# Optimization experiments

Measured on AMD Instinct MI355X. Metric: run time of the kernel, lower is better.

Reference implementation:

```python
import jax, jax.numpy as jnp
import numpy as np

P, H_OUT, D, NX = 32, 1, 256, 16
S_A = -0.1

def layernorm(x, g, b, eps=1e-5):
    mu = jnp.mean(x, axis=-1, keepdims=True)
    var = jnp.var(x, axis=-1, keepdims=True)
    return (x - mu) * jax.lax.rsqrt(var + eps) * g + b

def setup_inputs() -> dict:
    key = jax.random.key(0)
    ks = jax.random.split(key, 16)
    B, L = 8, 2048
    y = jax.random.normal(ks[0], (B, L, P), jnp.float32)
    Win = jax.random.normal(ks[1], (P, D), jnp.float32) / np.sqrt(P)
    bin_ = jnp.zeros((D,), jnp.float32)
    ng = jnp.ones((D,), jnp.float32); nb = jnp.zeros((D,), jnp.float32)
    # A = -10*rand + s_A, with A[:,0] = s_A (fix first state of each channel)
    A = -10.0 * jax.random.uniform(ks[2], (D, NX), jnp.float32) + S_A
    A = A.at[:, 0].set(S_A)
    W_B = jax.random.normal(ks[3], (NX, D), jnp.float32)
    W_C = jax.random.normal(ks[4], (NX, D), jnp.float32)
    q_delta = jax.random.normal(ks[5], (D,), jnp.float32)
    p_delta = jax.random.normal(ks[6], (1,), jnp.float32)
    nfg = jnp.ones((D,), jnp.float32); nfb = jnp.zeros((D,), jnp.float32)
    W1 = jax.random.normal(ks[7], (D, D), jnp.float32) / np.sqrt(D)
    b1 = jnp.zeros((D,), jnp.float32)
    W2 = jax.random.normal(ks[8], (D, H_OUT * P), jnp.float32) / np.sqrt(D)
    b2 = jnp.zeros((H_OUT * P,), jnp.float32)
    return {"y": y, "Win": Win, "bin_": bin_, "ng": ng, "nb": nb, "A": A,
            "W_B": W_B, "W_C": W_C, "q_delta": q_delta, "p_delta": p_delta,
            "nfg": nfg, "nfb": nfb, "W1": W1, "b1": b1, "W2": W2, "b2": b2}

def selective_scan(u, delta, A, Bm, Cm):
    # u: (B,L,D), delta: (B,L), A: (D,NX), Bm/Cm: (B,L,NX)
    dA = jnp.exp(delta[..., None, None] * A)                      # (B,L,D,NX)
    dBu = delta[..., None, None] * Bm[:, :, None, :] * u[..., None]  # (B,L,D,NX)
    x0 = jnp.zeros((u.shape[0], u.shape[2], A.shape[1]), u.dtype)
    def step(x, inp):
        dA_t, dBu_t, C_t = inp
        x = dA_t * x + dBu_t                                      # (B,D,NX)
        y_t = jnp.einsum('bdn,bn->bd', x, C_t)
        return x, y_t
    _, ys = jax.lax.scan(step, x0, (dA.transpose(1, 0, 2, 3),
                                    dBu.transpose(1, 0, 2, 3),
                                    Cm.transpose(1, 0, 2)))
    return ys.transpose(1, 0, 2)                                  # (B,L,D)

def reference(y, Win, bin_, ng, nb, A, W_B, W_C, q_delta, p_delta,
              nfg, nfb, W1, b1, W2, b2):
    B, L, _ = y.shape
    h = y @ Win + bin_                                            # (B,L,D)
    hn = layernorm(h, ng, nb)
    delta = jax.nn.softplus(p_delta[0] + jnp.einsum('bld,d->bl', hn, q_delta))
    Bm = jnp.einsum('nd,bld->bln', W_B, hn)
    Cm = jnp.einsum('nd,bld->bln', W_C, hn)
    upd = selective_scan(hn, delta, A, Bm, Cm)
    h = h + upd
    h = layernorm(h, nfg, nfb)
    out = jax.nn.gelu(h @ W1 + b1, approximate=False) @ W2 + b2
    return out.reshape(B, L, H_OUT, P)
```

## Files before the change

### kernel.cpp

```cpp
#include <hip/hip_runtime.h>
#include <math.h>

#define D 256
#define NX 16
#define L 2048
#define NBATCH 8
#define NTOK (NBATCH * L)
#define CL 32
#define NCH (L / CL)
#define LOG2E 1.44269504088896340736f

typedef float f32x4 __attribute__((ext_vector_type(4)));
typedef short bf16x8 __attribute__((ext_vector_type(8)));

__device__ __forceinline__ unsigned short f2bf(float x) {
  unsigned u = __float_as_uint(x);
  u = u + 0x7fffu + ((u >> 16) & 1u);
  return (unsigned short)(u >> 16);
}
__device__ __forceinline__ float bf2f(unsigned short h) {
  return __uint_as_float(((unsigned)h) << 16);
}

__global__ __launch_bounds__(256) void k0_prep(const float* __restrict__ A,
                                               const float* __restrict__ WB,
                                               const float* __restrict__ WC,
                                               const float* __restrict__ Win,
                                               const float* __restrict__ W1,
                                               const float* __restrict__ W2,
                                               float* __restrict__ At,
                                               unsigned short* __restrict__ W1fh,
                                               unsigned short* __restrict__ W1fl,
                                               unsigned short* __restrict__ W2fh,
                                               unsigned short* __restrict__ W2fl,
                                               unsigned short* __restrict__ Winfh,
                                               unsigned short* __restrict__ Winfl,
                                               unsigned short* __restrict__ Wbcfh,
                                               unsigned short* __restrict__ Wbcfl) {
  int i = blockIdx.x * 256 + threadIdx.x;
  if (i < 4096) {
    int d = i >> 4, n = i & 15;
    At[n * D + d] = A[i] * LOG2E;
  } else if (i < 12288) {
    int e = i - 4096;
    int j = e & 7, l = (e >> 3) & 63, tt = e >> 9;
    int k = ((l >> 4) << 3) + j;
    int n = tt * 16 + (l & 15);
    float x = Win[k * 256 + n];
    unsigned short h = f2bf(x);
    Winfh[e] = h;
    Winfl[e] = f2bf(x - bf2f(h));
  } else if (i < 20480) {
    int e = i - 12288;
    int j = e & 7, l = (e >> 3) & 63, q = e >> 9;
    int s = q >> 1, tt = q & 1;
    int k = s * 32 + ((l >> 4) << 3) + j;
    int n = tt * 16 + (l & 15);
    float x = (n < 16) ? WB[n * 256 + k] : WC[(n - 16) * 256 + k];
    unsigned short h = f2bf(x);
    Wbcfh[e] = h;
    Wbcfl[e] = f2bf(x - bf2f(h));
  } else if (i < 86016) {
    int e = i - 20480;
    int j = e & 7, l = (e >> 3) & 63, tt = (e >> 9) & 15, s = e >> 13;
    int k = s * 32 + ((l >> 4) << 3) + j;
    int n = tt * 16 + (l & 15);
    float x = W1[k * 256 + n];
    unsigned short h = f2bf(x);
    W1fh[e] = h;
    W1fl[e] = f2bf(x - bf2f(h));
  } else {
    int e = i - 86016;
    int j = e & 7, l = (e >> 3) & 63, tt = (e >> 9) & 1, s = e >> 10;
    int k = s * 32 + ((l >> 4) << 3) + j;
    int n = tt * 16 + (l & 15);
    float x = W2[k * 32 + n];
    unsigned short h = f2bf(x);
    W2fh[e] = h;
    W2fl[e] = f2bf(x - bf2f(h));
  }
}

__global__ __launch_bounds__(512, 4) void k1a_front_scan(
    const float* __restrict__ y, const float* __restrict__ bin_,
    const float* __restrict__ ng, const float* __restrict__ nb,
    const float* __restrict__ qd, const float* __restrict__ pd,
    const float* __restrict__ At,
    const unsigned short* __restrict__ Winfh,
    const unsigned short* __restrict__ Winfl,
    const unsigned short* __restrict__ Wbcfh,
    const unsigned short* __restrict__ Wbcfl,
    float* __restrict__ hn, float* __restrict__ delta,
    float* __restrict__ Bm, float* __restrict__ Cm,
    float* __restrict__ muv, float* __restrict__ irsv,
    float* __restrict__ EX, float* __restrict__ T) {
  __shared__ float sy[32][36];
  __shared__ float sh[32][260];
  __shared__ float sB[32][NX];
  __shared__ float sred[32][16];
  __shared__ float sdelta[32];
  __shared__ float smu[32];
  __shared__ float srstd[32];
  __shared__ __align__(16) unsigned short sChA_h[32 * 256];
  __shared__ __align__(16) unsigned short sChA_l[32 * 256];
  int t = threadIdx.x;
  int l = t & 63;
  int w = t >> 6;
  int tok0 = blockIdx.x * 32;
  if (t < 256) {
    int row = t >> 3, c4 = t & 7;
    *(float4*)&sy[row][c4 * 4] = ((const float4*)(y + (size_t)tok0 * 32))[t];
  }
  __syncthreads();
  f32x4 acc[2][2];
  {
    bf16x8 yah[2], yal[2];
    int k0 = (l >> 4) << 3;
    #pragma unroll
    for (int m = 0; m < 2; ++m) {
      int row = m * 16 + (l & 15);
      float4 f0 = *(float4*)&sy[row][k0];
      float4 f1 = *(float4*)&sy[row][k0 + 4];
      float v0 = f0.x, v1_ = f0.y, v2 = f0.z, v3 = f0.w;
      float v4 = f1.x, v5 = f1.y, v6 = f1.z, v7 = f1.w;
      unsigned short h0 = f2bf(v0), h1 = f2bf(v1_), h2 = f2bf(v2), h3 = f2bf(v3);
      unsigned short h4 = f2bf(v4), h5 = f2bf(v5), h6 = f2bf(v6), h7 = f2bf(v7);
      yah[m][0] = (short)h0; yah[m][1] = (short)h1; yah[m][2] = (short)h2; yah[m][3] = (short)h3;
      yah[m][4] = (short)h4; yah[m][5] = (short)h5; yah[m][6] = (short)h6; yah[m][7] = (short)h7;
      yal[m][0] = (short)f2bf(v0 - bf2f(h0)); yal[m][1] = (short)f2bf(v1_ - bf2f(h1));
      yal[m][2] = (short)f2bf(v2 - bf2f(h2)); yal[m][3] = (short)f2bf(v3 - bf2f(h3));
      yal[m][4] = (short)f2bf(v4 - bf2f(h4)); yal[m][5] = (short)f2bf(v5 - bf2f(h5));
      yal[m][6] = (short)f2bf(v6 - bf2f(h6)); yal[m][7] = (short)f2bf(v7 - bf2f(h7));
    }
    const bf16x8* Bh = (const bf16x8*)Winfh;
    const bf16x8* Bl = (const bf16x8*)Winfl;
    #pragma unroll
    for (int n = 0; n < 2; ++n) {
      int tt = w * 2 + n;
      bf16x8 bh = Bh[tt * 64 + l];
      bf16x8 bl = Bl[tt * 64 + l];
      #pragma unroll
      for (int m = 0; m < 2; ++m) {
        f32x4 a = {0.f, 0.f, 0.f, 0.f};
        a = __builtin_amdgcn_mfma_f32_16x16x32_bf16(yah[m], bh, a, 0, 0, 0);
        a = __builtin_amdgcn_mfma_f32_16x16x32_bf16(yal[m], bh, a, 0, 0, 0);
        a = __builtin_amdgcn_mfma_f32_16x16x32_bf16(yah[m], bl, a, 0, 0, 0);
        a = __builtin_amdgcn_mfma_f32_16x16x32_bf16(yal[m], bl, a, 0, 0, 0);
        acc[m][n] = a;
      }
    }
  }
  int c0 = w * 32 + (l & 15), c1 = c0 + 16;
  {
    float b0 = bin_[c0], b1v = bin_[c1];
    #pragma unroll
    for (int m = 0; m < 2; ++m)
      #pragma unroll
      for (int r = 0; r < 4; ++r) { acc[m][0][r] += b0; acc[m][1][r] += b1v; }
  }
  {
    #pragma unroll
    for (int m = 0; m < 2; ++m)
      #pragma unroll
      for (int r = 0; r < 4; ++r) {
        float a0 = acc[m][0][r], a1 = acc[m][1][r];
        float s1 = a0 + a1;
        float s2 = a0 * a0 + a1 * a1;
        #pragma unroll
        for (int off = 1; off < 16; off <<= 1) {
          s1 += __shfl_xor(s1, off);
          s2 += __shfl_xor(s2, off);
        }
        if ((l & 15) == 0) {
          int tok = m * 16 + ((l >> 4) << 2) + r;
          sred[tok][w * 2] = s1;
          sred[tok][w * 2 + 1] = s2;
        }
      }
  }
  __syncthreads();
  if (t < 32) {
    float s1 = 0.f, s2 = 0.f;
    #pragma unroll
    for (int q = 0; q < 8; ++q) { s1 += sred[t][q * 2]; s2 += sred[t][q * 2 + 1]; }
    float mu = s1 * (1.f / D);
    float var = s2 * (1.f / D) - mu * mu;
    float rstd = rsqrtf(var + 1e-5f);
    smu[t] = mu;
    srstd[t] = rstd;
    muv[tok0 + t] = mu;
    irsv[tok0 + t] = sqrtf(var + 1e-5f);
  }
  __syncthreads();
  {
    float g0 = ng[c0], g1 = ng[c1];
    float nb0 = nb[c0], nb1 = nb[c1];
    float q0 = qd[c0], q1 = qd[c1];
    float ddv[2][4];
    #pragma unroll
    for (int m = 0; m < 2; ++m)
      #pragma unroll
      for (int r = 0; r < 4; ++r) {
        int tok = m * 16 + ((l >> 4) << 2) + r;
        float mu = smu[tok], rstd = srstd[tok];
        float h0 = (acc[m][0][r] - mu) * rstd * g0 + nb0;
        float h1 = (acc[m][1][r] - mu) * rstd * g1 + nb1;
        sh[tok][c0] = h0;
        sh[tok][c1] = h1;
        float dx = h0 * q0 + h1 * q1;
        #pragma unroll
        for (int off = 1; off < 16; off <<= 1) dx += __shfl_xor(dx, off);
        ddv[m][r] = dx;
      }
    if ((l & 15) == 0) {
      #pragma unroll
      for (int m = 0; m < 2; ++m)
        #pragma unroll
        for (int r = 0; r < 4; ++r)
          sred[m * 16 + ((l >> 4) << 2) + r][w] = ddv[m][r];
    }
  }
  __syncthreads();
  if (t < 32) {
    float dsum = 0.f;
    #pragma unroll
    for (int q = 0; q < 8; ++q) dsum += sred[t][q];
    float xx = pd[0] + dsum;
    float dv = (xx > 20.f) ? xx : log1pf(expf(xx));
    delta[tok0 + t] = dv;
    sdelta[t] = dv;
    float tv = dv;
    #pragma unroll
    for (int off = 1; off < 32; off <<= 1) tv += __shfl_xor(tv, off);
    if (t == 0) T[blockIdx.x] = tv;
  }
  {
    int row = t & 31;
    int cq = (t >> 5) * 16;
    float4 f0 = *(float4*)&sh[row][cq];
    float4 f1 = *(float4*)&sh[row][cq + 4];
    float4 f2 = *(float4*)&sh[row][cq + 8];
    float4 f3 = *(float4*)&sh[row][cq + 12];
    float vv[16] = {f0.x, f0.y, f0.z, f0.w, f1.x, f1.y, f1.z, f1.w,
                    f2.x, f2.y, f2.z, f2.w, f3.x, f3.y, f3.z, f3.w};
    unsigned hw[8], lw[8];
    #pragma unroll
    for (int p = 0; p < 8; ++p) {
      unsigned short ha = f2bf(vv[2 * p]), hb = f2bf(vv[2 * p + 1]);
      unsigned short la = f2bf(vv[2 * p] - bf2f(ha));
      unsigned short lb = f2bf(vv[2 * p + 1] - bf2f(hb));
      hw[p] = (unsigned)ha | ((unsigned)hb << 16);
      lw[p] = (unsigned)la | ((unsigned)lb << 16);
    }
    unsigned base = (unsigned)row * 512;
    #pragma unroll
    for (int g = 0; g < 2; ++g) {
      unsigned off = ((unsigned)(cq * 2 + g * 16)) ^ ((unsigned)(row & 7) << 4);
      uint4 hv4 = {hw[g * 4], hw[g * 4 + 1], hw[g * 4 + 2], hw[g * 4 + 3]};
      uint4 lv4 = {lw[g * 4], lw[g * 4 + 1], lw[g * 4 + 2], lw[g * 4 + 3]};
      *(uint4*)((char*)sChA_h + base + off) = hv4;
      *(uint4*)((char*)sChA_l + base + off) = lv4;
    }
  }
  __syncthreads();
  if (w < 4) {
    int mw = w & 1, nw = w >> 1;
    int row = mw * 16 + (l & 15);
    unsigned abase = (unsigned)row * 512;
    const bf16x8* B2h = (const bf16x8*)Wbcfh;
    const bf16x8* B2l = (const bf16x8*)Wbcfl;
    f32x4 acc2 = {0.f, 0.f, 0.f, 0.f};
    #pragma unroll
    for (int s = 0; s < 8; ++s) {
      unsigned off = ((unsigned)(s * 64 + ((l >> 4) << 4))) ^ ((unsigned)(row & 7) << 4);
      bf16x8 ah = *(const bf16x8*)((const char*)sChA_h + abase + off);
      bf16x8 al = *(const bf16x8*)((const char*)sChA_l + abase + off);
      int bi = (s * 2 + nw) * 64 + l;
      bf16x8 bh = B2h[bi];
      bf16x8 bl = B2l[bi];
      acc2 = __builtin_amdgcn_mfma_f32_16x16x32_bf16(ah, bh, acc2, 0, 0, 0);
      acc2 = __builtin_amdgcn_mfma_f32_16x16x32_bf16(al, bh, acc2, 0, 0, 0);
      acc2 = __builtin_amdgcn_mfma_f32_16x16x32_bf16(ah, bl, acc2, 0, 0, 0);
      acc2 = __builtin_amdgcn_mfma_f32_16x16x32_bf16(al, bl, acc2, 0, 0, 0);
    }
    int tokr = mw * 16 + ((l >> 4) << 2);
    int colc = l & 15;
    if (nw == 0) {
      #pragma unroll
      for (int r = 0; r < 4; ++r) {
        Bm[(size_t)(tok0 + tokr + r) * NX + colc] = acc2[r];
        sB[tokr + r][colc] = acc2[r];
      }
    } else {
      #pragma unroll
      for (int r = 0; r < 4; ++r)
        Cm[(size_t)(tok0 + tokr + r) * NX + colc] = acc2[r];
    }
  } else {
    float4* dst = (float4*)(hn + (size_t)tok0 * D);
    for (int i = t - 256; i < 2048; i += 256) {
      int row = i >> 6, c4 = i & 63;
      dst[i] = *(float4*)&sh[row][c4 * 4];
    }
  }
  __syncthreads();
  {
    int half = t >> 8;
    int d = t & 255;
    float a8[8], x8[8];
    #pragma unroll
    for (int n = 0; n < 8; ++n) {
      a8[n] = At[(half * 8 + n) * D + d];
      x8[n] = 0.f;
    }
    for (int lo = 0; lo < CL; ++lo) {
      float dlt = sdelta[lo];
      float du = dlt * sh[lo][d];
      float Bv[8];
      *(float4*)&Bv[0] = *(float4*)&sB[lo][half * 8];
      *(float4*)&Bv[4] = *(float4*)&sB[lo][half * 8 + 4];
      #pragma unroll
      for (int n = 0; n < 8; ++n)
        x8[n] = fmaf(exp2f(dlt * a8[n]), x8[n], du * Bv[n]);
    }
    size_t exbase = (size_t)blockIdx.x * (NX * D) + d;
    #pragma unroll
    for (int n = 0; n < 8; ++n) EX[exbase + (half * 8 + n) * D] = x8[n];
  }
}

__global__ __launch_bounds__(64) void k2b_chunkscan(
    const float* __restrict__ At, const float* __restrict__ T,
    float* __restrict__ EX) {
  __shared__ float sT[NCH];
  int b = blockIdx.x >> 6;
  int rem = ((blockIdx.x & 63) << 6) | threadIdx.x;
  sT[threadIdx.x] = T[b * NCH + threadIdx.x];
  __syncthreads();
  float A2 = At[rem];
  size_t base = ((size_t)b << 18) + rem;
  float eq[8];
  #pragma unroll
  for (int j = 0; j < 8; ++j) eq[j] = EX[base + ((size_t)j << 12)];
  float x = 0.f;
  #pragma unroll 8
  for (int c = 0; c < NCH; ++c) {
    float e = eq[c & 7];
    if (c + 8 < NCH) eq[c & 7] = EX[base + ((size_t)(c + 8) << 12)];
    EX[base + ((size_t)c << 12)] = x;
    x = fmaf(exp2f(sT[c] * A2), x, e);
  }
}

__device__ __forceinline__ float gelu_exact(float x) {
  return 0.5f * x * (1.f + erff(x * 0.70710678118654752440f));
}

__global__ __launch_bounds__(256) void k2cd_scan_mlp(
    const float* __restrict__ hn, const float* __restrict__ delta,
    const float* __restrict__ Bm, const float* __restrict__ Cm,
    const float* __restrict__ At, const float* __restrict__ EX,
    const float* __restrict__ muv, const float* __restrict__ irsv,
    const float* __restrict__ ng, const float* __restrict__ nb,
    const float* __restrict__ nfg, const float* __restrict__ nfb,
    const unsigned short* __restrict__ W1fh, const unsigned short* __restrict__ W1fl,
    const unsigned short* __restrict__ W2fh, const unsigned short* __restrict__ W2fl,
    const float* __restrict__ b1, const float* __restrict__ b2,
    float* __restrict__ out) {
  __shared__ float s_az[32 * 260];
  __shared__ __align__(16) unsigned short sAh[32 * 256];
  __shared__ __align__(16) unsigned short sAl[32 * 256];
  __shared__ float sB[32][NX];
  __shared__ float sC[32][NX];
  __shared__ float sdelta[32];
  __shared__ float smu[32];
  __shared__ float sirs[32];
  int t = threadIdx.x;
  int tok0 = blockIdx.x * 32;
  size_t tokbase = (size_t)tok0;
  if (t < 32) {
    sdelta[t] = delta[tokbase + t];
    smu[t] = muv[tokbase + t];
    sirs[t] = irsv[tokbase + t];
  }
  for (int i = t; i < 32 * NX; i += 256) {
    ((float*)sB)[i] = Bm[tokbase * NX + i];
    ((float*)sC)[i] = Cm[tokbase * NX + i];
  }
  float a16[16], x16[16];
  size_t exbase = (size_t)blockIdx.x * (NX * D) + t;
  #pragma unroll
  for (int n = 0; n < 16; ++n) {
    a16[n] = At[n * D + t];
    x16[n] = EX[exbase + n * D];
  }
  float nb_d = nb[t];
  float invg = 1.0f / ng[t];
  __syncthreads();
  {
    float hv = hn[tokbase * D + t];
    for (int lo = 0; lo < CL; ++lo) {
      float hv_next = (lo + 1 < CL) ? hn[(tokbase + lo + 1) * D + t] : 0.f;
      float dlt = sdelta[lo];
      float du = dlt * hv;
      float Bv[16], Cv[16];
      *(float4*)&Bv[0]  = *(float4*)&sB[lo][0];
      *(float4*)&Bv[4]  = *(float4*)&sB[lo][4];
      *(float4*)&Bv[8]  = *(float4*)&sB[lo][8];
      *(float4*)&Bv[12] = *(float4*)&sB[lo][12];
      *(float4*)&Cv[0]  = *(float4*)&sC[lo][0];
      *(float4*)&Cv[4]  = *(float4*)&sC[lo][4];
      *(float4*)&Cv[8]  = *(float4*)&sC[lo][8];
      *(float4*)&Cv[12] = *(float4*)&sC[lo][12];
      float p = 0.f;
      #pragma unroll
      for (int n = 0; n < 16; ++n) {
        x16[n] = fmaf(exp2f(dlt * a16[n]), x16[n], du * Bv[n]);
        p = fmaf(x16[n], Cv[n], p);
      }
      float h = fmaf((hv - nb_d) * invg, sirs[lo], smu[lo]);
      s_az[lo * 260 + t] = h + p;
      hv = hv_next;
    }
  }
  __syncthreads();
  int dcol = t & 63, jrow = t >> 6;
  int d4 = dcol * 4, j8 = jrow * 8;
  {
    float4 g4 = ((const float4*)nfg)[dcol];
    float4 b4 = ((const float4*)nfb)[dcol];
    for (int jj = 0; jj < 8; ++jj) {
      int lo = j8 + jj;
      float4 v = *(float4*)&s_az[lo * 260 + d4];
      float s1 = v.x + v.y + v.z + v.w;
      float s2 = v.x * v.x + v.y * v.y + v.z * v.z + v.w * v.w;
      #pragma unroll
      for (int off = 1; off < 64; off <<= 1) {
        s1 += __shfl_xor(s1, off);
        s2 += __shfl_xor(s2, off);
      }
      float mu2 = s1 * (1.f / D);
      float var2 = s2 * (1.f / D) - mu2 * mu2;
      float rstd2 = rsqrtf(var2 + 1e-5f);
      float4 o;
      o.x = (v.x - mu2) * rstd2 * g4.x + b4.x;
      o.y = (v.y - mu2) * rstd2 * g4.y + b4.y;
      o.z = (v.z - mu2) * rstd2 * g4.z + b4.z;
      o.w = (v.w - mu2) * rstd2 * g4.w + b4.w;
      unsigned short h0 = f2bf(o.x), h1 = f2bf(o.y), h2 = f2bf(o.z), h3 = f2bf(o.w);
      unsigned short q0 = f2bf(o.x - bf2f(h0));
      unsigned short q1 = f2bf(o.y - bf2f(h1));
      unsigned short q2 = f2bf(o.z - bf2f(h2));
      unsigned short q3 = f2bf(o.w - bf2f(h3));
      unsigned off16 = ((unsigned)(d4 * 2)) ^ ((unsigned)(lo & 7) << 4);
      uint2 hv2, lv2;
      hv2.x = (unsigned)h0 | ((unsigned)h1 << 16);
      hv2.y = (unsigned)h2 | ((unsigned)h3 << 16);
      lv2.x = (unsigned)q0 | ((unsigned)q1 << 16);
      lv2.y = (unsigned)q2 | ((unsigned)q3 << 16);
      *(uint2*)((char*)sAh + lo * 512 + off16) = hv2;
      *(uint2*)((char*)sAl + lo * 512 + off16) = lv2;
    }
  }
  __syncthreads();
  int l = t & 63, w = t >> 6;
  const bf16x8* B1h = (const bf16x8*)W1fh;
  const bf16x8* B1l = (const bf16x8*)W1fl;
  f32x4 acc[2][4];
  #pragma unroll
  for (int m = 0; m < 2; ++m)
    #pragma unroll
    for (int n = 0; n < 4; ++n) {
      f32x4 z4 = {0.f, 0.f, 0.f, 0.f};
      acc[m][n] = z4;
    }
  #pragma unroll 2
  for (int s = 0; s < 8; ++s) {
    bf16x8 ah[2], al[2];
    #pragma unroll
    for (int m = 0; m < 2; ++m) {
      int row = m * 16 + (l & 15);
      unsigned off16 = ((unsigned)(s * 64 + ((l >> 4) << 4))) ^ ((unsigned)(row & 7) << 4);
      ah[m] = *(const bf16x8*)((const char*)sAh + row * 512 + off16);
      al[m] = *(const bf16x8*)((const char*)sAl + row * 512 + off16);
    }
    #pragma unroll
    for (int n = 0; n < 4; ++n) {
      int bi = (s * 16 + w * 4 + n) * 64 + l;
      bf16x8 bh = B1h[bi];
      bf16x8 bl = B1l[bi];
      #pragma unroll
      for (int m = 0; m < 2; ++m) {
        acc[m][n] = __builtin_amdgcn_mfma_f32_16x16x32_bf16(ah[m], bh, acc[m][n], 0, 0, 0);
        acc[m][n] = __builtin_amdgcn_mfma_f32_16x16x32_bf16(al[m], bh, acc[m][n], 0, 0, 0);
        acc[m][n] = __builtin_amdgcn_mfma_f32_16x16x32_bf16(ah[m], bl, acc[m][n], 0, 0, 0);
        acc[m][n] = __builtin_amdgcn_mfma_f32_16x16x32_bf16(al[m], bl, acc[m][n], 0, 0, 0);
      }
    }
  }
  __syncthreads();
  #pragma unroll
  for (int n = 0; n < 4; ++n) {
    int colz = w * 64 + n * 16 + (l & 15);
    float b1v = b1[colz];
    #pragma unroll
    for (int m = 0; m < 2; ++m) {
      #pragma unroll
      for (int r = 0; r < 4; ++r) {
        int row = m * 16 + ((l >> 4) << 2) + r;
        float zv = gelu_exact(acc[m][n][r] + b1v);
        unsigned short zh = f2bf(zv);
        unsigned short zl = f2bf(zv - bf2f(zh));
        unsigned off16 = ((unsigned)(colz * 2)) ^ ((unsigned)(row & 7) << 4);
        *(unsigned short*)((char*)sAh + row * 512 + off16) = zh;
        *(unsigned short*)((char*)sAl + row * 512 + off16) = zl;
      }
    }
  }
  __syncthreads();
  int mw = w >> 1, nw = w & 1;
  const bf16x8* B2h = (const bf16x8*)W2fh;
  const bf16x8* B2l = (const bf16x8*)W2fl;
  f32x4 acc2 = {0.f, 0.f, 0.f, 0.f};
  #pragma unroll 2
  for (int s = 0; s < 8; ++s) {
    int row = mw * 16 + (l & 15);
    unsigned off16 = ((unsigned)(s * 64 + ((l >> 4) << 4))) ^ ((unsigned)(row & 7) << 4);
    bf16x8 zh8 = *(const bf16x8*)((const char*)sAh + row * 512 + off16);
    bf16x8 zl8 = *(const bf16x8*)((const char*)sAl + row * 512 + off16);
    int bi = (s * 2 + nw) * 64 + l;
    bf16x8 bh = B2h[bi];
    bf16x8 bl = B2l[bi];
    acc2 = __builtin_amdgcn_mfma_f32_16x16x32_bf16(zh8, bh, acc2, 0, 0, 0);
    acc2 = __builtin_amdgcn_mfma_f32_16x16x32_bf16(zl8, bh, acc2, 0, 0, 0);
    acc2 = __builtin_amdgcn_mfma_f32_16x16x32_bf16(zh8, bl, acc2, 0, 0, 0);
    acc2 = __builtin_amdgcn_mfma_f32_16x16x32_bf16(zl8, bl, acc2, 0, 0, 0);
  }
  int colo = nw * 16 + (l & 15);
  float b2v = b2[colo];
  #pragma unroll
  for (int r = 0; r < 4; ++r) {
    int row = mw * 16 + ((l >> 4) << 2) + r;
    out[(size_t)(tok0 + row) * 32 + colo] = acc2[r] + b2v;
  }
}

extern "C" void kernel_launch(void* const* d_in, const int* in_sizes, int n_in,
                              void* d_out, int out_size, void* d_ws, size_t ws_size,
                              hipStream_t stream) {
  const float* y    = (const float*)d_in[0];
  const float* Win  = (const float*)d_in[1];
  const float* bin_ = (const float*)d_in[2];
  const float* ng   = (const float*)d_in[3];
  const float* nb   = (const float*)d_in[4];
  const float* A    = (const float*)d_in[5];
  const float* WB   = (const float*)d_in[6];
  const float* WC   = (const float*)d_in[7];
  const float* qd   = (const float*)d_in[8];
  const float* pd   = (const float*)d_in[9];
  const float* nfg  = (const float*)d_in[10];
  const float* nfb  = (const float*)d_in[11];
  const float* W1   = (const float*)d_in[12];
  const float* b1   = (const float*)d_in[13];
  const float* W2   = (const float*)d_in[14];
  const float* b2   = (const float*)d_in[15];

  float* ws = (float*)d_ws;
  float* hnbuf = ws;
  float* delta = ws + 4194304;
  float* Bm    = delta + NTOK;
  float* Cm    = Bm + NTOK * NX;
  float* muv   = Cm + NTOK * NX;
  float* irsv  = muv + NTOK;
  float* Tbuf  = irsv + NTOK;
  float* At    = Tbuf + NBATCH * NCH;
  float* EX    = At + D * NX;
  unsigned short* W1fh  = (unsigned short*)(EX + 2097152);
  unsigned short* W1fl  = W1fh + 65536;
  unsigned short* W2fh  = W1fl + 65536;
  unsigned short* W2fl  = W2fh + 8192;
  unsigned short* Winfh = W2fl + 8192;
  unsigned short* Winfl = Winfh + 8192;
  unsigned short* Wbcfh = Winfl + 8192;
  unsigned short* Wbcfl = Wbcfh + 8192;

  k0_prep<<<368, 256, 0, stream>>>(A, WB, WC, Win, W1, W2, At,
                                   W1fh, W1fl, W2fh, W2fl,
                                   Winfh, Winfl, Wbcfh, Wbcfl);
  k1a_front_scan<<<NTOK / 32, 512, 0, stream>>>(y, bin_, ng, nb, qd, pd, At,
                                                Winfh, Winfl, Wbcfh, Wbcfl,
                                                hnbuf, delta, Bm, Cm,
                                                muv, irsv, EX, Tbuf);
  k2b_chunkscan<<<NBATCH * 64, 64, 0, stream>>>(At, Tbuf, EX);
  k2cd_scan_mlp<<<NTOK / 32, 256, 0, stream>>>(hnbuf, delta, Bm, Cm, At, EX,
                                               muv, irsv, ng, nb, nfg, nfb,
                                               W1fh, W1fl, W2fh, W2fl,
                                               b1, b2, (float*)d_out);
}
```

Baseline: 185.3 us.

## Split scan+MLP kernel into 16-token half-chunks using mid-chunk partial states

The front kernel now also writes the intra-chunk scan state after 16 tokens (EXmid) and a prefix sum of delta up to token 15 (cds15). The scan+MLP kernel runs on 16-token half-chunks, so it launches twice as many blocks, each with half the serial scan length. The second half reconstructs its starting state from the chunk carry plus the mid-chunk partial. This is meant to shorten the serial per-block scan and raise occupancy (launch bounds 256,4). In exchange it adds an extra 8MB EXmid write and read, duplicates the A/EX loads across two blocks, and leaves two of the four waves idle in the second GEMM.

Measured after the change: 180.8 us (median of 2 runs). 2.4% less time.

```diff
diff --git a/kernel.cpp b/kernel.cpp
--- a/kernel.cpp
+++ b/kernel.cpp
@@ -93,7 +93,8 @@
     float* __restrict__ hn, float* __restrict__ delta,
     float* __restrict__ Bm, float* __restrict__ Cm,
     float* __restrict__ muv, float* __restrict__ irsv,
-    float* __restrict__ EX, float* __restrict__ T) {
+    float* __restrict__ EX, float* __restrict__ EXmid,
+    float* __restrict__ cds15g, float* __restrict__ T) {
   __shared__ float sy[32][36];
   __shared__ float sh[32][260];
   __shared__ float sB[32][NX];
@@ -229,10 +230,14 @@
     float dv = (xx > 20.f) ? xx : log1pf(expf(xx));
     delta[tok0 + t] = dv;
     sdelta[t] = dv;
-    float tv = dv;
-    #pragma unroll
-    for (int off = 1; off < 32; off <<= 1) tv += __shfl_xor(tv, off);
-    if (t == 0) T[blockIdx.x] = tv;
+    float c = dv;
+    #pragma unroll
+    for (int off = 1; off < 32; off <<= 1) {
+      float o = __shfl_up(c, off);
+      if (t >= off) c += o;
+    }
+    if (t == 15) cds15g[blockIdx.x] = c;
+    if (t == 31) T[blockIdx.x] = c;
   }
   {
     int row = t & 31;
@@ -313,7 +318,8 @@
       a8[n] = At[(half * 8 + n) * D + d];
       x8[n] = 0.f;
     }
-    for (int lo = 0; lo < CL; ++lo) {
+    size_t exbase = (size_t)blockIdx.x * (NX * D) + d;
+    for (int lo = 0; lo < 16; ++lo) {
       float dlt = sdelta[lo];
       float du = dlt * sh[lo][d];
       float Bv[8];
@@ -323,7 +329,18 @@
       for (int n = 0; n < 8; ++n)
         x8[n] = fmaf(exp2f(dlt * a8[n]), x8[n], du * Bv[n]);
     }
-    size_t exbase = (size_t)blockIdx.x * (NX * D) + d;
+    #pragma unroll
+    for (int n = 0; n < 8; ++n) EXmid[exbase + (half * 8 + n) * D] = x8[n];
+    for (int lo = 16; lo < 32; ++lo) {
+      float dlt = sdelta[lo];
+      float du = dlt * sh[lo][d];
+      float Bv[8];
+      *(float4*)&Bv[0] = *(float4*)&sB[lo][half * 8];
+      *(float4*)&Bv[4] = *(float4*)&sB[lo][half * 8 + 4];
+      #pragma unroll
+      for (int n = 0; n < 8; ++n)
+        x8[n] = fmaf(exp2f(dlt * a8[n]), x8[n], du * Bv[n]);
+    }
     #pragma unroll
     for (int n = 0; n < 8; ++n) EX[exbase + (half * 8 + n) * D] = x8[n];
   }
@@ -356,10 +373,11 @@
   return 0.5f * x * (1.f + erff(x * 0.70710678118654752440f));
 }
 
-__global__ __launch_bounds__(256) void k2cd_scan_mlp(
+__global__ __launch_bounds__(256, 4) void k2cd_scan_mlp(
     const float* __restrict__ hn, const float* __restrict__ delta,
     const float* __restrict__ Bm, const float* __restrict__ Cm,
     const float* __restrict__ At, const float* __restrict__ EX,
+    const float* __restrict__ EXmid, const float* __restrict__ cds15g,
     const float* __restrict__ muv, const float* __restrict__ irsv,
     const float* __restrict__ ng, const float* __restrict__ nb,
     const float* __restrict__ nfg, const float* __restrict__ nfb,
@@ -367,40 +385,46 @@
     const unsigned short* __restrict__ W2fh, const unsigned short* __restrict__ W2fl,
     const float* __restrict__ b1, const float* __restrict__ b2,
     float* __restrict__ out) {
-  __shared__ float s_az[32 * 260];
-  __shared__ __align__(16) unsigned short sAh[32 * 256];
-  __shared__ __align__(16) unsigned short sAl[32 * 256];
-  __shared__ float sB[32][NX];
-  __shared__ float sC[32][NX];
-  __shared__ float sdelta[32];
-  __shared__ float smu[32];
-  __shared__ float sirs[32];
+  __shared__ float s_az[16 * 260];
+  __shared__ __align__(16) unsigned short sAh[16 * 256];
+  __shared__ __align__(16) unsigned short sAl[16 * 256];
+  __shared__ float sB[16][NX];
+  __shared__ float sC[16][NX];
+  __shared__ float sdelta[16];
+  __shared__ float smu[16];
+  __shared__ float sirs[16];
   int t = threadIdx.x;
-  int tok0 = blockIdx.x * 32;
+  int chunk = blockIdx.x >> 1;
+  int half = blockIdx.x & 1;
+  int tok0 = blockIdx.x * 16;
   size_t tokbase = (size_t)tok0;
-  if (t < 32) {
+  if (t < 16) {
     sdelta[t] = delta[tokbase + t];
     smu[t] = muv[tokbase + t];
     sirs[t] = irsv[tokbase + t];
   }
-  for (int i = t; i < 32 * NX; i += 256) {
-    ((float*)sB)[i] = Bm[tokbase * NX + i];
-    ((float*)sC)[i] = Cm[tokbase * NX + i];
-  }
+  ((float*)sB)[t] = Bm[tokbase * NX + t];
+  ((float*)sC)[t] = Cm[tokbase * NX + t];
   float a16[16], x16[16];
-  size_t exbase = (size_t)blockIdx.x * (NX * D) + t;
+  size_t exbase = (size_t)chunk * (NX * D) + t;
   #pragma unroll
   for (int n = 0; n < 16; ++n) {
     a16[n] = At[n * D + t];
     x16[n] = EX[exbase + n * D];
   }
+  if (half) {
+    float c15 = cds15g[chunk];
+    #pragma unroll
+    for (int n = 0; n < 16; ++n)
+      x16[n] = fmaf(exp2f(c15 * a16[n]), x16[n], EXmid[exbase + n * D]);
+  }
   float nb_d = nb[t];
   float invg = 1.0f / ng[t];
   __syncthreads();
   {
     float hv = hn[tokbase * D + t];
-    for (int lo = 0; lo < CL; ++lo) {
-      float hv_next = (lo + 1 < CL) ? hn[(tokbase + lo + 1) * D + t] : 0.f;
+    for (int lo = 0; lo < 16; ++lo) {
+      float hv_next = (lo + 1 < 16) ? hn[(tokbase + lo + 1) * D + t] : 0.f;
       float dlt = sdelta[lo];
       float du = dlt * hv;
       float Bv[16], Cv[16];
@@ -425,12 +449,12 @@
   }
   __syncthreads();
   int dcol = t & 63, jrow = t >> 6;
-  int d4 = dcol * 4, j8 = jrow * 8;
+  int d4 = dcol * 4, j4 = jrow * 4;
   {
     float4 g4 = ((const float4*)nfg)[dcol];
     float4 b4 = ((const float4*)nfb)[dcol];
-    for (int jj = 0; jj < 8; ++jj) {
-      int lo = j8 + jj;
+    for (int jj = 0; jj < 4; ++jj) {
+      int lo = j4 + jj;
       float4 v = *(float4*)&s_az[lo * 260 + d4];
       float s1 = v.x + v.y + v.z + v.w;
       float s2 = v.x * v.x + v.y * v.y + v.z * v.z + v.w * v.w;
@@ -466,36 +490,27 @@
   int l = t & 63, w = t >> 6;
   const bf16x8* B1h = (const bf16x8*)W1fh;
   const bf16x8* B1l = (const bf16x8*)W1fl;
-  f32x4 acc[2][4];
+  f32x4 acc[4];
   #pragma unroll
-  for (int m = 0; m < 2; ++m)
-    #pragma unroll
-    for (int n = 0; n < 4; ++n) {
-      f32x4 z4 = {0.f, 0.f, 0.f, 0.f};
-      acc[m][n] = z4;
-    }
+  for (int n = 0; n < 4; ++n) {
+    f32x4 z4 = {0.f, 0.f, 0.f, 0.f};
+    acc[n] = z4;
+  }
   #pragma unroll 2
   for (int s = 0; s < 8; ++s) {
-    bf16x8 ah[2], al[2];
-    #pragma unroll
-    for (int m = 0; m < 2; ++m) {
-      int row = m * 16 + (l & 15);
-      unsigned off16 = ((unsigned)(s * 64 + ((l >> 4) << 4))) ^ ((unsigned)(row & 7) << 4);
-      ah[m] = *(const bf16x8*)((const char*)sAh + row * 512 + off16);
-      al[m] = *(const bf16x8*)((const char*)sAl + row * 512 + off16);
-    }
+    int row = l & 15;
+    unsigned off16 = ((unsigned)(s * 64 + ((l >> 4) << 4))) ^ ((unsigned)(row & 7) << 4);
+    bf16x8 ah = *(const bf16x8*)((const char*)sAh + row * 512 + off16);
+    bf16x8 al = *(const bf16x8*)((const char*)sAl + row * 512 + off16);
     #pragma unroll
     for (int n = 0; n < 4; ++n) {
       int bi = (s * 16 + w * 4 + n) * 64 + l;
       bf16x8 bh = B1h[bi];
       bf16x8 bl = B1l[bi];
-      #pragma unroll
-      for (int m = 0; m < 2; ++m) {
-        acc[m][n] = __builtin_amdgcn_mfma_f32_16x16x32_bf16(ah[m], bh, acc[m][n], 0, 0, 0);
-        acc[m][n] = __builtin_amdgcn_mfma_f32_16x16x32_bf16(al[m], bh, acc[m][n], 0, 0, 0);
-        acc[m][n] = __builtin_amdgcn_mfma_f32_16x16x32_bf16(ah[m], bl, acc[m][n], 0, 0, 0);
-        acc[m][n] = __builtin_amdgcn_mfma_f32_16x16x32_bf16(al[m], bl, acc[m][n], 0, 0, 0);
-      }
+      acc[n] = __builtin_amdgcn_mfma_f32_16x16x32_bf16(ah, bh, acc[n], 0, 0, 0);
+      acc[n] = __builtin_amdgcn_mfma_f32_16x16x32_bf16(al, bh, acc[n], 0, 0, 0);
+      acc[n] = __builtin_amdgcn_mfma_f32_16x16x32_bf16(ah, bl, acc[n], 0, 0, 0);
+      acc[n] = __builtin_amdgcn_mfma_f32_16x16x32_bf16(al, bl, acc[n], 0, 0, 0);
     }
   }
   __syncthreads();
@@ -504,44 +519,43 @@
     int colz = w * 64 + n * 16 + (l & 15);
     float b1v = b1[colz];
     #pragma unroll
-    for (int m = 0; m < 2; ++m) {
-      #pragma unroll
-      for (int r = 0; r < 4; ++r) {
-        int row = m * 16 + ((l >> 4) << 2) + r;
-        float zv = gelu_exact(acc[m][n][r] + b1v);
-        unsigned short zh = f2bf(zv);
-        unsigned short zl = f2bf(zv - bf2f(zh));
-        unsigned off16 = ((unsigned)(colz * 2)) ^ ((unsigned)(row & 7) << 4);
-        *(unsigned short*)((char*)sAh + row * 512 + off16) = zh;
-        *(unsigned short*)((char*)sAl + row * 512 + off16) = zl;
-      }
-    }
-  }
-  __syncthreads();
-  int mw = w >> 1, nw = w & 1;
-  const bf16x8* B2h = (const bf16x8*)W2fh;
-  const bf16x8* B2l = (const bf16x8*)W2fl;
-  f32x4 acc2 = {0.f, 0.f, 0.f, 0.f};
-  #pragma unroll 2
-  for (int s = 0; s < 8; ++s) {
-    int row = mw * 16 + (l & 15);
-    unsigned off16 = ((unsigned)(s * 64 + ((l >> 4) << 4))) ^ ((unsigned)(row & 7) << 4);
-    bf16x8 zh8 = *(const bf16x8*)((const char*)sAh + row * 512 + off16);
-    bf16x8 zl8 = *(const bf16x8*)((const char*)sAl + row * 512 + off16);
-    int bi = (s * 2 + nw) * 64 + l;
-    bf16x8 bh = B2h[bi];
-    bf16x8 bl = B2l[bi];
-    acc2 = __builtin_amdgcn_mfma_f32_16x16x32_bf16(zh8, bh, acc2, 0, 0, 0);
-    acc2 = __builtin_amdgcn_mfma_f32_16x16x32_bf16(zl8, bh, acc2, 0, 0, 0);
-    acc2 = __builtin_amdgcn_mfma_f32_16x16x32_bf16(zh8, bl, acc2, 0, 0, 0);
-    acc2 = __builtin_amdgcn_mfma_f32_16x16x32_bf16(zl8, bl, acc2, 0, 0, 0);
-  }
-  int colo = nw * 16 + (l & 15);
-  float b2v = b2[colo];
-  #pragma unroll
-  for (int r = 0; r < 4; ++r) {
-    int row = mw * 16 + ((l >> 4) << 2) + r;
-    out[(size_t)(tok0 + row) * 32 + colo] = acc2[r] + b2v;
+    for (int r = 0; r < 4; ++r) {
+      int row = ((l >> 4) << 2) + r;
+      float zv = gelu_exact(acc[n][r] + b1v);
+      unsigned short zh = f2bf(zv);
+      unsigned short zl = f2bf(zv - bf2f(zh));
+      unsigned off16 = ((unsigned)(colz * 2)) ^ ((unsigned)(row & 7) << 4);
+      *(unsigned short*)((char*)sAh + row * 512 + off16) = zh;
+      *(unsigned short*)((char*)sAl + row * 512 + off16) = zl;
+    }
+  }
+  __syncthreads();
+  if (w < 2) {
+    int nw = w;
+    const bf16x8* B2h = (const bf16x8*)W2fh;
+    const bf16x8* B2l = (const bf16x8*)W2fl;
+    f32x4 acc2 = {0.f, 0.f, 0.f, 0.f};
+    #pragma unroll 2
+    for (int s = 0; s < 8; ++s) {
+      int row = l & 15;
+      unsigned off16 = ((unsigned)(s * 64 + ((l >> 4) << 4))) ^ ((unsigned)(row & 7) << 4);
+      bf16x8 zh8 = *(const bf16x8*)((const char*)sAh + row * 512 + off16);
+      bf16x8 zl8 = *(const bf16x8*)((const char*)sAl + row * 512 + off16);
+      int bi = (s * 2 + nw) * 64 + l;
+      bf16x8 bh = B2h[bi];
+      bf16x8 bl = B2l[bi];
+      acc2 = __builtin_amdgcn_mfma_f32_16x16x32_bf16(zh8, bh, acc2, 0, 0, 0);
+      acc2 = __builtin_amdgcn_mfma_f32_16x16x32_bf16(zl8, bh, acc2, 0, 0, 0);
+      acc2 = __builtin_amdgcn_mfma_f32_16x16x32_bf16(zh8, bl, acc2, 0, 0, 0);
+      acc2 = __builtin_amdgcn_mfma_f32_16x16x32_bf16(zl8, bl, acc2, 0, 0, 0);
+    }
+    int colo = nw * 16 + (l & 15);
+    float b2v = b2[colo];
+    #pragma unroll
+    for (int r = 0; r < 4; ++r) {
+      int row = ((l >> 4) << 2) + r;
+      out[(size_t)(tok0 + row) * 32 + colo] = acc2[r] + b2v;
+    }
   }
 }
 
@@ -573,9 +587,11 @@
   float* muv   = Cm + NTOK * NX;
   float* irsv  = muv + NTOK;
   float* Tbuf  = irsv + NTOK;
-  float* At    = Tbuf + NBATCH * NCH;
+  float* cds15 = Tbuf + NBATCH * NCH;
+  float* At    = cds15 + NBATCH * NCH;
   float* EX    = At + D * NX;
-  unsigned short* W1fh  = (unsigned short*)(EX + 2097152);
+  float* EXmid = EX + 2097152;
+  unsigned short* W1fh  = (unsigned short*)(EXmid + 2097152);
   unsigned short* W1fl  = W1fh + 65536;
   unsigned short* W2fh  = W1fl + 65536;
   unsigned short* W2fl  = W2fh + 8192;
@@ -590,9 +606,11 @@
   k1a_front_scan<<<NTOK / 32, 512, 0, stream>>>(y, bin_, ng, nb, qd, pd, At,
                                                 Winfh, Winfl, Wbcfh, Wbcfl,
                                                 hnbuf, delta, Bm, Cm,
-                                                muv, irsv, EX, Tbuf);
+                                                muv, irsv, EX, EXmid,
+                                                cds15, Tbuf);
   k2b_chunkscan<<<NBATCH * 64, 64, 0, stream>>>(At, Tbuf, EX);
-  k2cd_scan_mlp<<<NTOK / 32, 256, 0, stream>>>(hnbuf, delta, Bm, Cm, At, EX,
+  k2cd_scan_mlp<<<NTOK / 16, 256, 0, stream>>>(hnbuf, delta, Bm, Cm, At, EX,
+                                               EXmid, cds15,
                                                muv, irsv, ng, nb, nfg, nfb,
                                                W1fh, W1fl, W2fh, W2fl,
                                                b1, b2, (float*)d_out);
```
